# Kernel tuning notes

Measured on AMD Instinct MI355X. Metric: run time of the kernel, lower is better.

## Reference

```python
import jax, jax.numpy as jnp
import numpy as np

B, S, H, DH, E = 8, 2048, 1024, 4096, 8
ALPHA = 0.5
LN_EPS = 1e-5


def setup_inputs() -> dict:
    key = jax.random.key(0)
    ks = jax.random.split(key, 8)
    sc = 0.02
    return {
        "x": jax.random.normal(ks[0], (B, S, H), jnp.float32),
        "We1": jax.random.normal(ks[1], (E, H, DH), jnp.float32) * sc,
        "be1": jnp.zeros((E, DH), jnp.float32),
        "We2": jax.random.normal(ks[2], (E, DH, H), jnp.float32) * sc,
        "be2": jnp.zeros((E, H), jnp.float32),
        "Wq": jax.random.normal(ks[3], (H, H), jnp.float32) * sc,
        "bq": jnp.zeros((H,), jnp.float32),
        "Wk": jax.random.normal(ks[4], (H, H), jnp.float32) * sc,
        "bk": jnp.zeros((H,), jnp.float32),
        "Wv": jax.random.normal(ks[5], (H, H), jnp.float32) * sc,
        "bv": jnp.zeros((H,), jnp.float32),
        "ln_g": jnp.ones((H,), jnp.float32),
        "ln_b": jnp.zeros((H,), jnp.float32),
        "current_expert_idx": E - 1,
    }


def _boosting_forward(x, We1, be1, We2, be2, Wq, bq, Wk, bk, Wv, bv, ln_g, ln_b, cur):
    sg = jax.lax.stop_gradient
    n = cur + 1  # static Python int: number of experts executed
    boost = sg(x)  # boost_input = x.detach()
    outs = []
    for i in range(n):
        h = jax.nn.relu(jnp.einsum("bsh,hf->bsf", boost, We1[i]) + be1[i])
        eo = jnp.einsum("bsf,fh->bsh", h, We2[i]) + be2[i]  # dropout = identity (eval)
        if i < n - 1:
            eo = sg(eo)  # earlier experts detached
        boost = boost + ALPHA * eo
        outs.append(eo)
    stacked = jnp.stack(outs, axis=2)  # [B,S,n,H]
    q = jnp.einsum("bsh,hd->bsd", x, Wq) + bq          # [B,S,H]
    k = jnp.einsum("bseh,hd->bsed", stacked, Wk) + bk  # [B,S,n,H]
    v = jnp.einsum("bseh,hd->bsed", stacked, Wv) + bv
    scores = jnp.einsum("bsd,bsed->bse", q, k) / jnp.sqrt(jnp.asarray(H, x.dtype))
    w = jax.nn.softmax(scores, axis=-1)                # [B,S,n]
    fused = jnp.einsum("bse,bsed->bsd", w, v)          # [B,S,H]
    y = x + fused
    mu = jnp.mean(y, axis=-1, keepdims=True)
    var = jnp.mean(jnp.square(y - mu), axis=-1, keepdims=True)
    return (y - mu) * jax.lax.rsqrt(var + LN_EPS) * ln_g + ln_b


def reference(x, We1, be1, We2, be2, Wq, bq, Wk, bk, Wv, bv, ln_g, ln_b, current_expert_idx):
    return _boosting_forward(x, We1, be1, We2, be2, Wq, bq, Wk, bk, Wv, bv, ln_g, ln_b, int(current_expert_idx))
```

## Files before the change

### kernel.cpp

```cpp
#include <hip/hip_runtime.h>
#include <math.h>

typedef __bf16 bf16_t;
typedef __bf16 bf16x8 __attribute__((ext_vector_type(8)));
typedef __bf16 bf16x4 __attribute__((ext_vector_type(4)));
typedef float f32x4 __attribute__((ext_vector_type(4)));
typedef unsigned int u32;

static constexpr int kBd = 8, kS = 2048, kH = 1024, kDH = 4096, kE = 8;
static constexpr int kM = kBd * kS;
static constexpr float kScale = 0.03125f;

__device__ __forceinline__ void gload_lds16(const void* g, void* l) {
  __builtin_amdgcn_global_load_lds(
      (const __attribute__((address_space(1))) u32*)g,
      (__attribute__((address_space(3))) u32*)l, 16, 0, 0);
}

__global__ __launch_bounds__(256) void cvt_flat_kernel(const float* __restrict__ in,
                                                       bf16_t* __restrict__ out, int n4) {
  int i = blockIdx.x * 256 + threadIdx.x;
  if (i >= n4) return;
  f32x4 v = *(const f32x4*)(in + (size_t)i * 4);
  bf16x4 o;
#pragma unroll
  for (int j = 0; j < 4; ++j) o[j] = (bf16_t)v[j];
  *(bf16x4*)(out + (size_t)i * 4) = o;
}

__global__ __launch_bounds__(256) void transpose_cvt_kernel(
    const float* __restrict__ in, bf16_t* __restrict__ out, int R, int C) {
  __shared__ float tile[32][33];
  int tx = threadIdx.x & 31, ty = threadIdx.x >> 5;
  int c0 = blockIdx.x * 32, r0 = blockIdx.y * 32;
#pragma unroll
  for (int yy = 0; yy < 4; ++yy)
    tile[ty + yy * 8][tx] = in[(size_t)(r0 + ty + yy * 8) * C + c0 + tx];
  __syncthreads();
#pragma unroll
  for (int yy = 0; yy < 4; ++yy)
    out[(size_t)(c0 + ty + yy * 8) * R + r0 + tx] = (bf16_t)tile[tx][ty + yy * 8];
}

template <int MODE>
__global__ __launch_bounds__(512, 2) void gemm256_kernel(
    const bf16_t* __restrict__ A, const bf16_t* __restrict__ Bt,
    int M, int N, int K, int nwg,
    const float* __restrict__ bias,
    bf16_t* __restrict__ outb,
    const float* __restrict__ bin_f, float* __restrict__ bout_f,
    const bf16_t* __restrict__ bin_b, bf16_t* __restrict__ bout_b,
    bf16_t* __restrict__ stacked,
    const float* __restrict__ xres, float* __restrict__ yout,
    const int* __restrict__ curp, int expert_i) {
  if ((MODE == 0 || MODE == 1 || MODE == 4) && expert_i > *curp) return;
  extern __shared__ char lds_buf[];
  char* Abase = lds_buf;
  char* Bbase = lds_buf + 98304;
  const int tid = threadIdx.x;
  const int lane = tid & 63, wid = tid >> 6;
  const int wr = wid >> 2, wc = wid & 3;
  const int fr = lane & 15, fh = lane >> 4;
  const int lane_swz = (fr * 64 + fh * 16) ^ ((fr >> 3) << 5);
  const int bid = blockIdx.x;
  const int wg = (bid & 7) * (nwg >> 3) + (bid >> 3);
  const int nMb = M >> 8;
  const int m0 = (wg % nMb) << 8, n0 = (wg / nMb) << 8;
  int grow[2], gcol[2];
#pragma unroll
  for (int j = 0; j < 2; ++j) {
    int L = (j * 512 + tid) * 16;
    int Lp = L ^ (((L >> 9) & 1) << 5);
    int s = Lp >> 10;
    grow[j] = ((s >> 1) << 4) + ((Lp >> 6) & 15);
    gcol[j] = ((s & 1) << 5) + (((Lp >> 4) & 3) << 3);
  }
  const bf16_t* sA[2] = {A + (size_t)(m0 + grow[0]) * K + gcol[0],
                         A + (size_t)(m0 + grow[1]) * K + gcol[1]};
  const bf16_t* sB[2] = {Bt + (size_t)(n0 + grow[0]) * K + gcol[0],
                         Bt + (size_t)(n0 + grow[1]) * K + gcol[1]};
  const size_t rstep = (size_t)128 * K;

#define STAGE(SP, BASE, tau, h)                                               \
  {                                                                           \
    char* d_ = (BASE) + ((h) << 14) + (wid << 10);                            \
    gload_lds16(SP[0] + (size_t)(h)*rstep + (size_t)(tau)*64, d_);            \
    gload_lds16(SP[1] + (size_t)(h)*rstep + (size_t)(tau)*64, d_ + 8192);     \
  }
#define STAGE_A(buf, t, h) STAGE(sA, Abase + (buf)*32768, (t), (h))
#define STAGE_B(t, h) STAGE(sB, Bbase + (((t)&1) << 15), (t), (h))
#define SB0() __builtin_amdgcn_sched_barrier(0)

  const int bq = (wc & 1) * 4;

  f32x4 acc[8][4] = {};
  const int NT = K >> 6;

#define QUAD(p, af)                                                            \
  __builtin_amdgcn_s_setprio(1);                                               \
  _Pragma("unroll") for (int nf = 0; nf < 4; ++nf) {                           \
    acc[2 * (p)][nf] = __builtin_amdgcn_mfma_f32_16x16x32_bf16(                \
        af[0], b[nf][0], acc[2 * (p)][nf], 0, 0, 0);                           \
    acc[2 * (p)][nf] = __builtin_amdgcn_mfma_f32_16x16x32_bf16(                \
        af[1], b[nf][1], acc[2 * (p)][nf], 0, 0, 0);                           \
    acc[2 * (p) + 1][nf] = __builtin_amdgcn_mfma_f32_16x16x32_bf16(            \
        af[2], b[nf][0], acc[2 * (p) + 1][nf], 0, 0, 0);                       \
    acc[2 * (p) + 1][nf] = __builtin_amdgcn_mfma_f32_16x16x32_bf16(            \
        af[3], b[nf][1], acc[2 * (p) + 1][nf], 0, 0, 0);                       \
  }                                                                            \
  __builtin_amdgcn_s_setprio(0);

  STAGE_A(0, 0, 0); STAGE_A(0, 0, 1);
  STAGE_B(0, 0); STAGE_B(0, 1);
  STAGE_A(1, 1, 0); STAGE_A(1, 1, 1);
  STAGE_B(1, 0); STAGE_B(1, 1);
  asm volatile("s_waitcnt vmcnt(8)" ::: "memory");
  __builtin_amdgcn_s_barrier();

  int am0 = 0;
  for (int t = 0; t < NT; ++t) {
    int am2 = am0 + 2; if (am2 >= 3) am2 -= 3;
    const char* Ar = Abase + am0 * 32768 + (wr << 14) + lane_swz;
    const char* Br = Bbase + ((t & 1) << 15) + ((wc >> 1) << 14) + lane_swz;
    bf16x8 b[4][2], a01[8], a23[8];
    const bool st = (t + 2 < NT);
#pragma unroll
    for (int nf = 0; nf < 4; ++nf)
#pragma unroll
      for (int kk = 0; kk < 2; ++kk)
        b[nf][kk] = *(const bf16x8*)(Br + ((bq + nf) * 2 + kk) * 1024);
    SB0();
#pragma unroll
    for (int i = 0; i < 8; ++i) a01[i] = *(const bf16x8*)(Ar + i * 1024);
    SB0();
    if (st) { STAGE_A(am2, t + 2, 0); STAGE_A(am2, t + 2, 1); }
    SB0();
    QUAD(0, (&a01[0]));
#pragma unroll
    for (int i = 0; i < 8; ++i) a23[i] = *(const bf16x8*)(Ar + (8 + i) * 1024);
    SB0();
    QUAD(1, (&a01[4]));
    asm volatile("s_waitcnt lgkmcnt(8)" ::: "memory");
    SB0();
    if (st) { STAGE_B(t + 2, 0); STAGE_B(t + 2, 1); }
    SB0();
    QUAD(2, (&a23[0]));
    QUAD(3, (&a23[4]));
    if (t < NT - 2) {
      asm volatile("s_waitcnt vmcnt(8)" ::: "memory");
    } else {
      asm volatile("s_waitcnt vmcnt(0)" ::: "memory");
    }
    __builtin_amdgcn_s_barrier();
    am0 = am0 + 1; if (am0 >= 3) am0 -= 3;
  }
#undef QUAD
#undef STAGE
#undef STAGE_A
#undef STAGE_B
#undef SB0

#pragma unroll
  for (int nf = 0; nf < 4; ++nf) {
    const int col = n0 + wc * 64 + nf * 16 + fr;
    const float bv = bias ? bias[col] : 0.0f;
#pragma unroll
    for (int mf = 0; mf < 8; ++mf) {
#pragma unroll
      for (int r = 0; r < 4; ++r) {
        const int row = m0 + wr * 128 + mf * 16 + fh * 4 + r;
        const size_t idx = (size_t)row * N + col;
        float v = acc[mf][nf][r] + bv;
        if (MODE == 0) {
          outb[idx] = (bf16_t)(v > 0.0f ? v : 0.0f);
        } else if (MODE == 2) {
          outb[idx] = (bf16_t)v;
        } else if (MODE == 1) {
          float nb2 = bin_f[idx] + 0.5f * v;
          bout_f[idx] = nb2;
          bout_b[idx] = (bf16_t)nb2;
          stacked[idx] = (bf16_t)v;
        } else if (MODE == 4) {
          float nb2 = (float)bin_b[idx] + 0.5f * v;
          bout_b[idx] = (bf16_t)nb2;
          stacked[idx] = (bf16_t)v;
        } else {
          yout[idx] = v + xres[idx];
        }
      }
    }
  }
}

__global__ __launch_bounds__(256) void scores_mix_kernel(
    const bf16_t* __restrict__ qk, const bf16_t* __restrict__ q,
    const float* __restrict__ bk, const bf16_t* __restrict__ stacked,
    bf16_t* __restrict__ mix, const int* __restrict__ curp) {
  const int n = *curp + 1;
  int lane = threadIdx.x & 63, wave = threadIdx.x >> 6;
  int m = blockIdx.x * 4 + wave;
  size_t base = (size_t)m * kH + lane * 16;
  int c0 = lane * 16;
  bf16x8 qk0 = *(const bf16x8*)(qk + base);
  bf16x8 qk1 = *(const bf16x8*)(qk + base + 8);
  bf16x8 q0 = *(const bf16x8*)(q + base);
  bf16x8 q1 = *(const bf16x8*)(q + base + 8);
  float sc[kE + 1];
  bf16x8 eo0[kE], eo1[kE];
#pragma unroll
  for (int e = 0; e < kE; ++e) {
    sc[e] = 0.0f;
    if (e < n) {
      size_t sb = (size_t)e * kM * kH + base;
      eo0[e] = *(const bf16x8*)(stacked + sb);
      eo1[e] = *(const bf16x8*)(stacked + sb + 8);
      float d = 0.0f;
#pragma unroll
      for (int j = 0; j < 8; ++j)
        d += (float)eo0[e][j] * (float)qk0[j] + (float)eo1[e][j] * (float)qk1[j];
      sc[e] = d;
    }
  }
  {
    float qb = 0.0f;
#pragma unroll
    for (int j = 0; j < 8; ++j)
      qb += (float)q0[j] * bk[c0 + j] + (float)q1[j] * bk[c0 + 8 + j];
    sc[kE] = qb;
  }
#pragma unroll
  for (int off = 32; off >= 1; off >>= 1)
#pragma unroll
    for (int e = 0; e <= kE; ++e) sc[e] += __shfl_xor(sc[e], off, 64);
  float s[kE];
  float mx = -1e30f;
#pragma unroll
  for (int e = 0; e < kE; ++e)
    if (e < n) {
      s[e] = (sc[e] + sc[kE]) * kScale;
      mx = fmaxf(mx, s[e]);
    }
  float Z = 0.0f;
#pragma unroll
  for (int e = 0; e < kE; ++e)
    if (e < n) {
      s[e] = expf(s[e] - mx);
      Z += s[e];
    }
  float inv = 1.0f / Z;
  float mv[16];
#pragma unroll
  for (int j = 0; j < 16; ++j) mv[j] = 0.0f;
#pragma unroll
  for (int e = 0; e < kE; ++e)
    if (e < n) {
      float w = s[e] * inv;
#pragma unroll
      for (int j = 0; j < 8; ++j) {
        mv[j] += w * (float)eo0[e][j];
        mv[8 + j] += w * (float)eo1[e][j];
      }
    }
  bf16x8 o0, o1;
#pragma unroll
  for (int j = 0; j < 8; ++j) {
    o0[j] = (bf16_t)mv[j];
    o1[j] = (bf16_t)mv[8 + j];
  }
  *(bf16x8*)(mix + base) = o0;
  *(bf16x8*)(mix + base + 8) = o1;
}

__global__ __launch_bounds__(256) void layernorm_kernel(
    const float* __restrict__ y, const float* __restrict__ g,
    const float* __restrict__ b, float* __restrict__ out) {
  int lane = threadIdx.x & 63, wave = threadIdx.x >> 6;
  int m = blockIdx.x * 4 + wave;
  size_t base = (size_t)m * kH + lane * 16;
  f32x4 v[4];
#pragma unroll
  for (int j = 0; j < 4; ++j) v[j] = *(const f32x4*)(y + base + j * 4);
  float s = 0.0f, s2 = 0.0f;
#pragma unroll
  for (int j = 0; j < 4; ++j)
#pragma unroll
    for (int t = 0; t < 4; ++t) {
      float u = v[j][t];
      s += u;
      s2 += u * u;
    }
#pragma unroll
  for (int off = 32; off >= 1; off >>= 1) {
    s += __shfl_xor(s, off, 64);
    s2 += __shfl_xor(s2, off, 64);
  }
  float mu = s * (1.0f / kH);
  float var = s2 * (1.0f / kH) - mu * mu;
  float rs = rsqrtf(var + 1e-5f);
  int c0 = lane * 16;
#pragma unroll
  for (int j = 0; j < 4; ++j) {
    f32x4 gg = *(const f32x4*)(g + c0 + j * 4);
    f32x4 bb = *(const f32x4*)(b + c0 + j * 4);
    f32x4 o;
#pragma unroll
    for (int t = 0; t < 4; ++t) o[t] = (v[j][t] - mu) * rs * gg[t] + bb[t];
    *(f32x4*)(out + base + j * 4) = o;
  }
}

extern "C" void kernel_launch(void* const* d_in, const int* in_sizes, int n_in,
                              void* d_out, int out_size, void* d_ws, size_t ws_size,
                              hipStream_t stream) {
  const float* x = (const float*)d_in[0];
  const float* We1 = (const float*)d_in[1];
  const float* be1 = (const float*)d_in[2];
  const float* We2 = (const float*)d_in[3];
  const float* be2 = (const float*)d_in[4];
  const float* Wq = (const float*)d_in[5];
  const float* bq = (const float*)d_in[6];
  const float* Wk = (const float*)d_in[7];
  const float* bk = (const float*)d_in[8];
  const float* Wv = (const float*)d_in[9];
  const float* bv = (const float*)d_in[10];
  const float* ln_g = (const float*)d_in[11];
  const float* ln_b = (const float*)d_in[12];
  const int* curp = (const int*)d_in[13];
  float* out = (float*)d_out;

  char* ws = (char*)d_ws;
  const size_t MB = 1ull << 20;
  bf16_t* stacked = (bf16_t*)(ws);
  bf16_t* xb = (bf16_t*)(ws + 256 * MB);
  bf16_t* boostb = (bf16_t*)(ws + 288 * MB);
  bf16_t* wA = (bf16_t*)(ws + 320 * MB);
  bf16_t* wB = (bf16_t*)(ws + 328 * MB);
  bf16_t* WqT = (bf16_t*)(ws + 336 * MB);
  bf16_t* WkC = (bf16_t*)(ws + 338 * MB);
  bf16_t* WvT = (bf16_t*)(ws + 340 * MB);
  char* dyn = ws + 342 * MB;
  size_t rem = ws_size > 342 * MB ? ws_size - 342 * MB : 0;
  int nchunk;
  bool f32boost;
  if (rem >= 192 * MB) { nchunk = 1; f32boost = true; }
  else if (rem >= 128 * MB) { nchunk = 1; f32boost = false; }
  else if (rem >= 64 * MB) { nchunk = 2; f32boost = false; }
  else { nchunk = 4; f32boost = false; }
  bf16_t* hbuf = (bf16_t*)dyn;
  float* boostf = (float*)(dyn + 128 * MB);
  bf16_t* qb_ = hbuf;
  bf16_t* qkb = boostb;
  bf16_t* mixb = xb;
  float* yf = (float*)ws;

  const int Mc = kM / nchunk;
  const size_t MH = (size_t)kM * kH;
  const u32 kLds = 163840;
  dim3 blk(256), blk5(512);

  cvt_flat_kernel<<<(kM * kH) / 1024, blk, 0, stream>>>(x, xb, (kM * kH) / 4);
  cvt_flat_kernel<<<(kH * kH) / 1024, blk, 0, stream>>>(Wk, WkC, (kH * kH) / 4);
  transpose_cvt_kernel<<<dim3(kH / 32, kH / 32), blk, 0, stream>>>(Wq, WqT, kH, kH);
  transpose_cvt_kernel<<<dim3(kH / 32, kH / 32), blk, 0, stream>>>(Wv, WvT, kH, kH);

  for (int i = 0; i < kE; ++i) {
    transpose_cvt_kernel<<<dim3(kDH / 32, kH / 32), blk, 0, stream>>>(
        We1 + (size_t)i * kH * kDH, wA, kH, kDH);
    transpose_cvt_kernel<<<dim3(kH / 32, kDH / 32), blk, 0, stream>>>(
        We2 + (size_t)i * kH * kDH, wB, kDH, kH);
    for (int c = 0; c < nchunk; ++c) {
      const size_t ro = (size_t)c * Mc * kH;
      const bf16_t* Ain = ((i == 0) ? xb : boostb) + ro;
      {
        int nwg = (Mc / 256) * (kDH / 256);
        gemm256_kernel<0><<<nwg, blk5, kLds, stream>>>(
            Ain, wA, Mc, kDH, kH, nwg, be1 + (size_t)i * kDH, hbuf,
            nullptr, nullptr, nullptr, nullptr, nullptr, nullptr, nullptr, curp, i);
      }
      int nwg = (Mc / 256) * (kH / 256);
      if (f32boost) {
        const float* bin = ((i == 0) ? x : boostf) + ro;
        gemm256_kernel<1><<<nwg, blk5, kLds, stream>>>(
            hbuf, wB, Mc, kH, kDH, nwg, be2 + (size_t)i * kH, nullptr,
            bin, boostf + ro, nullptr, boostb + ro, stacked + (size_t)i * MH + ro,
            nullptr, nullptr, curp, i);
      } else {
        const bf16_t* binb = ((i == 0) ? xb : boostb) + ro;
        gemm256_kernel<4><<<nwg, blk5, kLds, stream>>>(
            hbuf, wB, Mc, kH, kDH, nwg, be2 + (size_t)i * kH, nullptr,
            nullptr, nullptr, binb, boostb + ro, stacked + (size_t)i * MH + ro,
            nullptr, nullptr, curp, i);
      }
    }
  }

  const int nwgH = (kM / 256) * (kH / 256);
  gemm256_kernel<2><<<nwgH, blk5, kLds, stream>>>(
      xb, WqT, kM, kH, kH, nwgH, bq, qb_,
      nullptr, nullptr, nullptr, nullptr, nullptr, nullptr, nullptr, curp, 0);
  gemm256_kernel<2><<<nwgH, blk5, kLds, stream>>>(
      qb_, WkC, kM, kH, kH, nwgH, nullptr, qkb,
      nullptr, nullptr, nullptr, nullptr, nullptr, nullptr, nullptr, curp, 0);
  scores_mix_kernel<<<dim3(kM / 4), blk, 0, stream>>>(qkb, qb_, bk, stacked, mixb, curp);
  gemm256_kernel<3><<<nwgH, blk5, kLds, stream>>>(
      mixb, WvT, kM, kH, kH, nwgH, bv, nullptr,
      nullptr, nullptr, nullptr, nullptr, nullptr, x, yf, curp, 0);
  layernorm_kernel<<<dim3(kM / 4), blk, 0, stream>>>(yf, ln_g, ln_b, out);
}
```

Before: 2.953 ms.

## Switch GEMM to 32x32x16 MFMA with a new swizzled LDS layout

Replaces the 16x16x32 bf16 MFMA tiling in the 256x256 GEMM with 32x32x16 MFMA instructions, so each wave holds 4x2 blocks of 16-float accumulators. The global-to-LDS staging layout and swizzle change to a row-major 128-byte-per-row layout with an XOR swizzle on 16-byte chunks, and the epilogue row/column mapping is rewritten to match. The aim is fewer MFMA issues and fewer LDS fragment reads per tile, lowering instruction overhead. It risks LDS bank conflicts if the new swizzle does not match the read pattern, and it changes scheduling relative to the existing waitcnt counts.

Result: slower. 3.462 ms (+17.2%).

```diff
diff --git a/kernel.cpp b/kernel.cpp
--- a/kernel.cpp
+++ b/kernel.cpp
@@ -5,6 +5,7 @@
 typedef __bf16 bf16x8 __attribute__((ext_vector_type(8)));
 typedef __bf16 bf16x4 __attribute__((ext_vector_type(4)));
 typedef float f32x4 __attribute__((ext_vector_type(4)));
+typedef float f32x16 __attribute__((ext_vector_type(16)));
 typedef unsigned int u32;
 
 static constexpr int kBd = 8, kS = 2048, kH = 1024, kDH = 4096, kE = 8;
@@ -60,25 +61,22 @@
   const int tid = threadIdx.x;
   const int lane = tid & 63, wid = tid >> 6;
   const int wr = wid >> 2, wc = wid & 3;
-  const int fr = lane & 15, fh = lane >> 4;
-  const int lane_swz = (fr * 64 + fh * 16) ^ ((fr >> 3) << 5);
+  const int l5 = lane & 31;
+  const int kxb = (lane >> 5) << 4;
+  const int sw = (lane & 7) << 4;
+  int kx[4];
+#pragma unroll
+  for (int ks = 0; ks < 4; ++ks) kx[ks] = ((ks << 5) + kxb) ^ sw;
   const int bid = blockIdx.x;
   const int wg = (bid & 7) * (nwg >> 3) + (bid >> 3);
   const int nMb = M >> 8;
   const int m0 = (wg % nMb) << 8, n0 = (wg / nMb) << 8;
-  int grow[2], gcol[2];
-#pragma unroll
-  for (int j = 0; j < 2; ++j) {
-    int L = (j * 512 + tid) * 16;
-    int Lp = L ^ (((L >> 9) & 1) << 5);
-    int s = Lp >> 10;
-    grow[j] = ((s >> 1) << 4) + ((Lp >> 6) & 15);
-    gcol[j] = ((s & 1) << 5) + (((Lp >> 4) & 3) << 3);
-  }
-  const bf16_t* sA[2] = {A + (size_t)(m0 + grow[0]) * K + gcol[0],
-                         A + (size_t)(m0 + grow[1]) * K + gcol[1]};
-  const bf16_t* sB[2] = {Bt + (size_t)(n0 + grow[0]) * K + gcol[0],
-                         Bt + (size_t)(n0 + grow[1]) * K + gcol[1]};
+  const int grow_ = tid >> 3;
+  const int gcol_ = (((tid & 7) ^ ((tid >> 3) & 7)) << 3);
+  const bf16_t* sA[2] = {A + (size_t)(m0 + grow_) * K + gcol_,
+                         A + (size_t)(m0 + grow_ + 64) * K + gcol_};
+  const bf16_t* sB[2] = {Bt + (size_t)(n0 + grow_) * K + gcol_,
+                         Bt + (size_t)(n0 + grow_ + 64) * K + gcol_};
   const size_t rstep = (size_t)128 * K;
 
 #define STAGE(SP, BASE, tau, h)                                               \
@@ -91,22 +89,16 @@
 #define STAGE_B(t, h) STAGE(sB, Bbase + (((t)&1) << 15), (t), (h))
 #define SB0() __builtin_amdgcn_sched_barrier(0)
 
-  const int bq = (wc & 1) * 4;
-
-  f32x4 acc[8][4] = {};
+  f32x16 acc[4][2] = {};
   const int NT = K >> 6;
 
-#define QUAD(p, af)                                                            \
+#define GROUP(g, AF, mi)                                                       \
   __builtin_amdgcn_s_setprio(1);                                               \
-  _Pragma("unroll") for (int nf = 0; nf < 4; ++nf) {                           \
-    acc[2 * (p)][nf] = __builtin_amdgcn_mfma_f32_16x16x32_bf16(                \
-        af[0], b[nf][0], acc[2 * (p)][nf], 0, 0, 0);                           \
-    acc[2 * (p)][nf] = __builtin_amdgcn_mfma_f32_16x16x32_bf16(                \
-        af[1], b[nf][1], acc[2 * (p)][nf], 0, 0, 0);                           \
-    acc[2 * (p) + 1][nf] = __builtin_amdgcn_mfma_f32_16x16x32_bf16(            \
-        af[2], b[nf][0], acc[2 * (p) + 1][nf], 0, 0, 0);                       \
-    acc[2 * (p) + 1][nf] = __builtin_amdgcn_mfma_f32_16x16x32_bf16(            \
-        af[3], b[nf][1], acc[2 * (p) + 1][nf], 0, 0, 0);                       \
+  _Pragma("unroll") for (int ks = 0; ks < 4; ++ks) {                           \
+    acc[g][0] = __builtin_amdgcn_mfma_f32_32x32x16_bf16(                       \
+        AF[mi][ks], b[0][ks], acc[g][0], 0, 0, 0);                             \
+    acc[g][1] = __builtin_amdgcn_mfma_f32_32x32x16_bf16(                       \
+        AF[mi][ks], b[1][ks], acc[g][1], 0, 0, 0);                             \
   }                                                                            \
   __builtin_amdgcn_s_setprio(0);
 
@@ -120,32 +112,38 @@
   int am0 = 0;
   for (int t = 0; t < NT; ++t) {
     int am2 = am0 + 2; if (am2 >= 3) am2 -= 3;
-    const char* Ar = Abase + am0 * 32768 + (wr << 14) + lane_swz;
-    const char* Br = Bbase + ((t & 1) << 15) + ((wc >> 1) << 14) + lane_swz;
-    bf16x8 b[4][2], a01[8], a23[8];
+    const char* ArL = Abase + am0 * 32768 + (wr << 14) + l5 * 128;
+    const char* BrL = Bbase + ((t & 1) << 15) + (wc << 13) + l5 * 128;
+    bf16x8 b[2][4], a01[2][4], a23[2][4];
     const bool st = (t + 2 < NT);
 #pragma unroll
-    for (int nf = 0; nf < 4; ++nf)
-#pragma unroll
-      for (int kk = 0; kk < 2; ++kk)
-        b[nf][kk] = *(const bf16x8*)(Br + ((bq + nf) * 2 + kk) * 1024);
-    SB0();
-#pragma unroll
-    for (int i = 0; i < 8; ++i) a01[i] = *(const bf16x8*)(Ar + i * 1024);
+    for (int nb = 0; nb < 2; ++nb)
+#pragma unroll
+      for (int ks = 0; ks < 4; ++ks)
+        b[nb][ks] = *(const bf16x8*)(BrL + nb * 4096 + kx[ks]);
+    SB0();
+#pragma unroll
+    for (int mb = 0; mb < 2; ++mb)
+#pragma unroll
+      for (int ks = 0; ks < 4; ++ks)
+        a01[mb][ks] = *(const bf16x8*)(ArL + mb * 4096 + kx[ks]);
     SB0();
     if (st) { STAGE_A(am2, t + 2, 0); STAGE_A(am2, t + 2, 1); }
     SB0();
-    QUAD(0, (&a01[0]));
-#pragma unroll
-    for (int i = 0; i < 8; ++i) a23[i] = *(const bf16x8*)(Ar + (8 + i) * 1024);
-    SB0();
-    QUAD(1, (&a01[4]));
+    GROUP(0, a01, 0);
+#pragma unroll
+    for (int mb = 0; mb < 2; ++mb)
+#pragma unroll
+      for (int ks = 0; ks < 4; ++ks)
+        a23[mb][ks] = *(const bf16x8*)(ArL + (2 + mb) * 4096 + kx[ks]);
+    SB0();
+    GROUP(1, a01, 1);
     asm volatile("s_waitcnt lgkmcnt(8)" ::: "memory");
     SB0();
     if (st) { STAGE_B(t + 2, 0); STAGE_B(t + 2, 1); }
     SB0();
-    QUAD(2, (&a23[0]));
-    QUAD(3, (&a23[4]));
+    GROUP(2, a23, 0);
+    GROUP(3, a23, 1);
     if (t < NT - 2) {
       asm volatile("s_waitcnt vmcnt(8)" ::: "memory");
     } else {
@@ -154,23 +152,24 @@
     __builtin_amdgcn_s_barrier();
     am0 = am0 + 1; if (am0 >= 3) am0 -= 3;
   }
-#undef QUAD
+#undef GROUP
 #undef STAGE
 #undef STAGE_A
 #undef STAGE_B
 #undef SB0
 
-#pragma unroll
-  for (int nf = 0; nf < 4; ++nf) {
-    const int col = n0 + wc * 64 + nf * 16 + fr;
+  const int rbase = (lane >> 5) << 2;
+#pragma unroll
+  for (int nb = 0; nb < 2; ++nb) {
+    const int col = n0 + wc * 64 + nb * 32 + l5;
     const float bv = bias ? bias[col] : 0.0f;
 #pragma unroll
-    for (int mf = 0; mf < 8; ++mf) {
-#pragma unroll
-      for (int r = 0; r < 4; ++r) {
-        const int row = m0 + wr * 128 + mf * 16 + fh * 4 + r;
+    for (int mb = 0; mb < 4; ++mb) {
+#pragma unroll
+      for (int reg = 0; reg < 16; ++reg) {
+        const int row = m0 + wr * 128 + mb * 32 + (reg & 3) + 8 * (reg >> 2) + rbase;
         const size_t idx = (size_t)row * N + col;
-        float v = acc[mf][nf][r] + bv;
+        float v = acc[mb][nb][reg] + bv;
         if (MODE == 0) {
           outb[idx] = (bf16_t)(v > 0.0f ? v : 0.0f);
         } else if (MODE == 2) {
```
